# Performance work log

Hardware: AMD Instinct MI355X
Metric: run time of the kernel (lower is better)

Reference implementation:

```python
import jax, jax.numpy as jnp
import numpy as np

B, L, D_BERT, D_PROJ, N_SPANS, HIDDEN, EXTRA = 128, 512, 1024, 64, 3, 512, 17
BN_EPS = 1e-5


def setup_inputs() -> dict:
    key = jax.random.key(0)
    ks = jax.random.split(key, 20)
    inp = {
        "bert_outputs": jax.random.normal(ks[0], (B, L, D_BERT), jnp.float32),
        "offsets": jnp.sort(jax.random.randint(ks[1], (B, N_SPANS, 2), 0, L), axis=-1),
        "in_urls": jax.random.uniform(ks[2], (B, 3), jnp.float32),
        "other_feats": jax.random.normal(ks[3], (B, 14), jnp.float32),
        # context conv (Conv1d: out=64, in=1024, k=3)
        "conv_w": jax.random.normal(ks[4], (D_PROJ, D_BERT, 3), jnp.float32) * 0.02,
        "conv_b": jnp.zeros((D_PROJ,), jnp.float32),
        # span extractor global attention Linear(64 -> 1)
        "att_w": jax.random.normal(ks[5], (D_PROJ,), jnp.float32) * 0.1,
        "att_b": jnp.zeros((), jnp.float32),
        # BatchNorm1d(192) in eval mode (running stats)
        "bn1_g": jnp.ones((D_PROJ * 3,), jnp.float32),
        "bn1_b": jnp.zeros((D_PROJ * 3,), jnp.float32),
        "bn1_m": jax.random.normal(ks[6], (D_PROJ * 3,), jnp.float32) * 0.1,
        "bn1_v": jax.random.uniform(ks[7], (D_PROJ * 3,), jnp.float32, 0.5, 1.5),
        # Linear(192 -> 512), kaiming
        "fc_w": jax.random.normal(ks[8], (HIDDEN, D_PROJ * 3), jnp.float32) * np.sqrt(2.0 / (D_PROJ * 3)),
        "fc_b": jnp.zeros((HIDDEN,), jnp.float32),
        # BatchNorm1d(512)
        "bn2_g": jnp.ones((HIDDEN,), jnp.float32),
        "bn2_b": jnp.zeros((HIDDEN,), jnp.float32),
        "bn2_m": jax.random.normal(ks[9], (HIDDEN,), jnp.float32) * 0.1,
        "bn2_v": jax.random.uniform(ks[10], (HIDDEN,), jnp.float32, 0.5, 1.5),
        # new_last_layer Linear(512+17 -> 3)
        "last_w": jax.random.normal(ks[11], (3, HIDDEN + EXTRA), jnp.float32) * 0.05,
        "last_b": jnp.zeros((3,), jnp.float32),
    }
    return inp


def _bn_eval(x, g, b, m, v):
    return (x - m) * jax.lax.rsqrt(v + BN_EPS) * g + b


def reference(bert_outputs, offsets, in_urls, other_feats, conv_w, conv_b,
              att_w, att_b, bn1_g, bn1_b, bn1_m, bn1_v, fc_w, fc_b,
              bn2_g, bn2_b, bn2_m, bn2_v, last_w, last_b):
    # Conv1d over sequence: [B,L,Dbert] -> [B,L,64], padding preserves length
    x = jnp.transpose(bert_outputs, (0, 2, 1))                      # [B, C_in, L]
    conv = jax.lax.conv_general_dilated(
        x, conv_w, window_strides=(1,), padding=[(1, 1)],
        dimension_numbers=("NCH", "OIH", "NCH"))
    conv = jnp.transpose(conv + conv_b[None, :, None], (0, 2, 1))   # [B, L, 64]

    # SelfAttentiveSpanExtractor: per-token logits, masked softmax within span, weighted sum
    logits = jnp.einsum("bld,d->bl", conv, att_w) + att_b           # [B, L]
    pos = jnp.arange(L)
    starts = offsets[..., 0][..., None]                             # [B, S, 1]
    ends = offsets[..., 1][..., None]
    span_mask = (pos[None, None, :] >= starts) & (pos[None, None, :] <= ends)  # [B,S,L]
    masked_logits = jnp.where(span_mask, logits[:, None, :], -1e9)
    attn = jax.nn.softmax(masked_logits, axis=-1)                   # [B, S, L]
    span_emb = jnp.einsum("bsl,bld->bsd", attn, conv)               # [B, S, 64]
    extracted = span_emb.reshape(span_emb.shape[0], -1)             # [B, 192]

    # fc: BN -> Linear -> ReLU -> BN -> Dropout(eval=identity)
    h = _bn_eval(extracted, bn1_g, bn1_b, bn1_m, bn1_v)
    h = jax.nn.relu(h @ fc_w.T + fc_b)
    h = _bn_eval(h, bn2_g, bn2_b, bn2_m, bn2_v)

    cat = jnp.concatenate([h, in_urls, other_feats], axis=1)        # [B, 529]
    return cat @ last_w.T + last_b                                  # [B, 3]
```

## Files before the change

### kernel.cpp

```cpp
#include <hip/hip_runtime.h>


typedef _Float16 f16x8 __attribute__((ext_vector_type(8)));
typedef _Float16 f16x4 __attribute__((ext_vector_type(4)));
typedef float    f32x16 __attribute__((ext_vector_type(16)));

#define B_      128
#define L_      512
#define DBERT   1024
#define DPROJ   64
#define NSPANS  3
#define HIDDEN  512
#define KSTEPS  32
#define BM      32
#define AROWS   34
#define ASTR    1032

__global__ __launch_bounds__(256)
void pack_w_kernel(const float* __restrict__ Wc, _Float16* __restrict__ Bp) {
    int idx = blockIdx.x * 256 + threadIdx.x;
    if (idx >= 384 * 64) return;
    int lane = idx & 63;
    int f    = idx >> 6;
    int ch   = f & 1;
    int ks   = (f >> 1) & 1;
    int t    = (f >> 2) % 3;
    int kb   = (f >> 2) / 3;
    int o     = ch * 32 + (lane & 31);
    int kbase = kb * 32 + ks * 16 + ((lane >> 5) << 3);
    f16x8 v;
    #pragma unroll
    for (int j = 0; j < 8; ++j)
        v[j] = (_Float16)Wc[(size_t)o * (DBERT * 3) + (size_t)(kbase + j) * 3 + t];
    *(f16x8*)(Bp + (size_t)idx * 8) = v;
}

__global__ __launch_bounds__(256, 2)
void conv_gemm_kernel(const float* __restrict__ X, const _Float16* __restrict__ Bp,
                      const float* __restrict__ cb, const float* __restrict__ aw,
                      const float* __restrict__ ab_p,
                      float* __restrict__ Y, float* __restrict__ Lg) {
    __shared__ __align__(16) char shraw[AROWS * ASTR * 2];
    __shared__ float loglds[2][BM];

    _Float16* As = (_Float16*)shraw;

    const int tid  = threadIdx.x;
    const int wv   = tid >> 6;
    const int lane = tid & 63;
    const int ch   = wv & 1;
    const int ks   = wv >> 1;
    const int m0   = blockIdx.x * BM;
    const int l0   = m0 & (L_ - 1);
    const int g0   = m0 - l0;

    f16x8 bcur[3], bnxt[3];
    #pragma unroll
    for (int t = 0; t < 3; ++t)
        bcur[t] = *(const f16x8*)(Bp + ((size_t)((t * 2 + ks) * 2 + ch) * 64 + lane) * 8);

    #pragma unroll
    for (int base = 0; base < 34; base += 8) {
        const int n = (base + 8 <= 34) ? 8 : (34 - base);
        float4 v[8];
        #pragma unroll
        for (int i = 0; i < 8; ++i) {
            if (i < n) {
                int l = l0 - 1 + base + i;
                v[i] = make_float4(0.f, 0.f, 0.f, 0.f);
                if (l >= 0 && l < L_)
                    v[i] = *(const float4*)(X + (size_t)(g0 + l) * DBERT + tid * 4);
            }
        }
        #pragma unroll
        for (int i = 0; i < 8; ++i) {
            if (i < n) {
                f16x4 h = {(_Float16)v[i].x, (_Float16)v[i].y,
                           (_Float16)v[i].z, (_Float16)v[i].w};
                *(f16x4*)(&As[(base + i) * ASTR + tid * 4]) = h;
            }
        }
    }
    __syncthreads();

    f32x16 acc = {};
    #pragma unroll 2
    for (int kb = 0; kb < KSTEPS; ++kb) {
        if (kb + 1 < KSTEPS) {
            #pragma unroll
            for (int t = 0; t < 3; ++t)
                bnxt[t] = *(const f16x8*)(
                    Bp + ((size_t)((((kb + 1) * 3 + t) * 2 + ks) * 2 + ch) * 64 + lane) * 8);
        }
        f16x8 afr[3];
        const int kboff = kb * 32 + ks * 16 + ((lane >> 5) << 3);
        #pragma unroll
        for (int t = 0; t < 3; ++t)
            afr[t] = *(const f16x8*)(&As[((lane & 31) + t) * ASTR + kboff]);
        #pragma unroll
        for (int t = 0; t < 3; ++t)
            acc = __builtin_amdgcn_mfma_f32_32x32x16_f16(afr[t], bcur[t], acc, 0, 0, 0);
        #pragma unroll
        for (int t = 0; t < 3; ++t) bcur[t] = bnxt[t];
    }

    __syncthreads();
    float* red = (float*)shraw;
    if (ks == 1) {
        #pragma unroll
        for (int i = 0; i < 16; ++i) red[(ch * 64 + lane) * 16 + i] = acc[i];
    }
    __syncthreads();
    if (ks == 0) {
        const int col = ch * 32 + (lane & 31);
        const float cbv = cb[col];
        const float awv = aw[col];
        const int rbase = (lane >> 5) << 2;
        #pragma unroll
        for (int i = 0; i < 16; ++i) {
            float c = acc[i] + red[(ch * 64 + lane) * 16 + i] + cbv;
            int row = (i & 3) + 8 * (i >> 2) + rbase;
            Y[(size_t)(m0 + row) * DPROJ + col] = c;
            float p = c * awv;
            p += __shfl_xor(p, 1);  p += __shfl_xor(p, 2);
            p += __shfl_xor(p, 4);  p += __shfl_xor(p, 8);
            p += __shfl_xor(p, 16);
            if ((lane & 31) == 0) loglds[ch][row] = p;
        }
    }
    __syncthreads();
    if (tid < BM)
        Lg[m0 + tid] = loglds[0][tid] + loglds[1][tid] + ab_p[0];
}

__global__ __launch_bounds__(256)
void span_emb_kernel(const float* __restrict__ conv, const float* __restrict__ Lg,
                     const int* __restrict__ offs, float* __restrict__ emb) {
    __shared__ float logits[L_];
    __shared__ float red[8];
    __shared__ float part[256];

    const int bs   = blockIdx.x;
    const int b    = bs / NSPANS;
    const int sp   = bs - b * NSPANS;
    const int tid  = threadIdx.x;
    const int lane = tid & 63;
    const int wv   = tid >> 6;

    if (tid < 128)
        *(float4*)(&logits[tid * 4]) = *(const float4*)(Lg + (size_t)b * L_ + tid * 4);
    __syncthreads();

    const int st = offs[b * (NSPANS * 2) + sp * 2 + 0];
    const int en = offs[b * (NSPANS * 2) + sp * 2 + 1];

    float mx = -1e30f;
    for (int l = st + tid; l <= en; l += 256) mx = fmaxf(mx, logits[l]);
    #pragma unroll
    for (int off = 32; off >= 1; off >>= 1) mx = fmaxf(mx, __shfl_xor(mx, off));
    if (lane == 0) red[wv] = mx;
    __syncthreads();
    mx = fmaxf(fmaxf(red[0], red[1]), fmaxf(red[2], red[3]));
    __syncthreads();

    float sm = 0.f;
    for (int l = st + tid; l <= en; l += 256) sm += __expf(logits[l] - mx);
    #pragma unroll
    for (int off = 32; off >= 1; off >>= 1) sm += __shfl_xor(sm, off);
    if (lane == 0) red[wv] = sm;
    __syncthreads();
    const float denom = red[0] + red[1] + red[2] + red[3];

    float a = 0.f;
    for (int l = st + wv; l <= en; l += 4)
        a += __expf(logits[l] - mx) * conv[((size_t)b * L_ + l) * DPROJ + lane];
    part[tid] = a;
    __syncthreads();
    if (tid < DPROJ)
        emb[(size_t)bs * DPROJ + tid] =
            (part[tid] + part[64 + tid] + part[128 + tid] + part[192 + tid]) / denom;
}

__global__ __launch_bounds__(256)
void span_fc_kernel(const float* __restrict__ emb_in,
                    const float* __restrict__ in_urls, const float* __restrict__ other,
                    const float* __restrict__ bn1_g, const float* __restrict__ bn1_b,
                    const float* __restrict__ bn1_m, const float* __restrict__ bn1_v,
                    const float* __restrict__ fc_w, const float* __restrict__ fc_b,
                    const float* __restrict__ bn2_g, const float* __restrict__ bn2_b,
                    const float* __restrict__ bn2_m, const float* __restrict__ bn2_v,
                    const float* __restrict__ last_w, const float* __restrict__ last_b,
                    float* __restrict__ out) {
    __shared__ float emb[NSPANS * DPROJ];
    __shared__ float hbuf[HIDDEN];

    const int b    = blockIdx.x;
    const int tid  = threadIdx.x;
    const int lane = tid & 63;
    const int wv   = tid >> 6;

    if (tid < NSPANS * DPROJ) {
        float e = emb_in[(size_t)b * (NSPANS * DPROJ) + tid];
        emb[tid] = (e - bn1_m[tid]) * rsqrtf(bn1_v[tid] + 1e-5f) * bn1_g[tid] + bn1_b[tid];
    }
    __syncthreads();

    #pragma unroll
    for (int q = 0; q < 2; ++q) {
        const int j = tid + q * 256;
        const float* wrow = fc_w + (size_t)j * (NSPANS * DPROJ);
        float s = fc_b[j];
        #pragma unroll 8
        for (int i = 0; i < NSPANS * DPROJ; ++i) s += wrow[i] * emb[i];
        s = fmaxf(s, 0.f);
        hbuf[j] = (s - bn2_m[j]) * rsqrtf(bn2_v[j] + 1e-5f) * bn2_g[j] + bn2_b[j];
    }
    __syncthreads();

    if (wv < 3) {
        const float* lw = last_w + wv * (HIDDEN + 17);
        float s = 0.f;
        for (int i = lane; i < HIDDEN + 17; i += 64) {
            float f;
            if (i < HIDDEN)          f = hbuf[i];
            else if (i < HIDDEN + 3) f = in_urls[b * 3 + (i - HIDDEN)];
            else                     f = other[b * 14 + (i - HIDDEN - 3)];
            s += lw[i] * f;
        }
        #pragma unroll
        for (int off = 32; off >= 1; off >>= 1) s += __shfl_xor(s, off);
        if (lane == 0) out[b * 3 + wv] = s + last_b[wv];
    }
}

extern "C" void kernel_launch(void* const* d_in, const int* in_sizes, int n_in,
                              void* d_out, int out_size, void* d_ws, size_t ws_size,
                              hipStream_t stream) {
    const float* bert    = (const float*)d_in[0];
    const int*   offs    = (const int*)d_in[1];
    const float* in_urls = (const float*)d_in[2];
    const float* other   = (const float*)d_in[3];
    const float* conv_w  = (const float*)d_in[4];
    const float* conv_b  = (const float*)d_in[5];
    const float* att_w   = (const float*)d_in[6];
    const float* att_b   = (const float*)d_in[7];
    const float* bn1_g   = (const float*)d_in[8];
    const float* bn1_b   = (const float*)d_in[9];
    const float* bn1_m   = (const float*)d_in[10];
    const float* bn1_v   = (const float*)d_in[11];
    const float* fc_w    = (const float*)d_in[12];
    const float* fc_b    = (const float*)d_in[13];
    const float* bn2_g   = (const float*)d_in[14];
    const float* bn2_b   = (const float*)d_in[15];
    const float* bn2_m   = (const float*)d_in[16];
    const float* bn2_v   = (const float*)d_in[17];
    const float* last_w  = (const float*)d_in[18];
    const float* last_b  = (const float*)d_in[19];

    _Float16* Bp      = (_Float16*)d_ws;
    float*    convout = (float*)((char*)d_ws + 393216);
    float*    logits  = (float*)((char*)d_ws + 393216 + (size_t)B_ * L_ * DPROJ * 4);
    float*    emb     = (float*)((char*)d_ws + 393216 + (size_t)B_ * L_ * DPROJ * 4 + 262144);

    hipLaunchKernelGGL(pack_w_kernel, dim3(96), dim3(256), 0, stream, conv_w, Bp);
    hipLaunchKernelGGL(conv_gemm_kernel, dim3((B_ * L_) / BM), dim3(256), 0, stream,
                       bert, Bp, conv_b, att_w, att_b, convout, logits);
    hipLaunchKernelGGL(span_emb_kernel, dim3(B_ * NSPANS), dim3(256), 0, stream,
                       convout, logits, offs, emb);
    hipLaunchKernelGGL(span_fc_kernel, dim3(B_), dim3(256), 0, stream,
                       emb, in_urls, other,
                       bn1_g, bn1_b, bn1_m, bn1_v, fc_w, fc_b,
                       bn2_g, bn2_b, bn2_m, bn2_v, last_w, last_b,
                       (float*)d_out);
}
```

Measured before the change: 152.1 us.

## Load conv GEMM A operands straight from global memory, dropping LDS staging

```diff
diff --git a/kernel.cpp b/kernel.cpp
--- a/kernel.cpp
+++ b/kernel.cpp
@@ -2,7 +2,6 @@
 
 
 typedef _Float16 f16x8 __attribute__((ext_vector_type(8)));
-typedef _Float16 f16x4 __attribute__((ext_vector_type(4)));
 typedef float    f32x16 __attribute__((ext_vector_type(16)));
 
 #define B_      128
@@ -11,10 +10,7 @@
 #define DPROJ   64
 #define NSPANS  3
 #define HIDDEN  512
-#define KSTEPS  32
-#define BM      32
-#define AROWS   34
-#define ASTR    1032
+#define KK      64
 
 __global__ __launch_bounds__(256)
 void pack_w_kernel(const float* __restrict__ Wc, _Float16* __restrict__ Bp) {
@@ -23,11 +19,10 @@
     int lane = idx & 63;
     int f    = idx >> 6;
     int ch   = f & 1;
-    int ks   = (f >> 1) & 1;
-    int t    = (f >> 2) % 3;
-    int kb   = (f >> 2) / 3;
+    int t    = (f >> 1) % 3;
+    int kk   = (f >> 1) / 3;
     int o     = ch * 32 + (lane & 31);
-    int kbase = kb * 32 + ks * 16 + ((lane >> 5) << 3);
+    int kbase = kk * 16 + ((lane >> 5) << 3);
     f16x8 v;
     #pragma unroll
     for (int j = 0; j < 8; ++j)
@@ -35,101 +30,86 @@
     *(f16x8*)(Bp + (size_t)idx * 8) = v;
 }
 
-__global__ __launch_bounds__(256, 2)
+__global__ __launch_bounds__(256, 4)
 void conv_gemm_kernel(const float* __restrict__ X, const _Float16* __restrict__ Bp,
                       const float* __restrict__ cb, const float* __restrict__ aw,
-                      const float* __restrict__ ab_p,
+                      const float* __restrict__ ab_p, const float* __restrict__ zp,
                       float* __restrict__ Y, float* __restrict__ Lg) {
-    __shared__ __align__(16) char shraw[AROWS * ASTR * 2];
-    __shared__ float loglds[2][BM];
-
-    _Float16* As = (_Float16*)shraw;
+    __shared__ float loglds[2][64];
 
     const int tid  = threadIdx.x;
     const int wv   = tid >> 6;
     const int lane = tid & 63;
+    const int rg   = wv >> 1;
     const int ch   = wv & 1;
-    const int ks   = wv >> 1;
-    const int m0   = blockIdx.x * BM;
+    const int m0   = blockIdx.x * 64;
     const int l0   = m0 & (L_ - 1);
     const int g0   = m0 - l0;
-
-    f16x8 bcur[3], bnxt[3];
-    #pragma unroll
-    for (int t = 0; t < 3; ++t)
-        bcur[t] = *(const f16x8*)(Bp + ((size_t)((t * 2 + ks) * 2 + ch) * 64 + lane) * 8);
-
-    #pragma unroll
-    for (int base = 0; base < 34; base += 8) {
-        const int n = (base + 8 <= 34) ? 8 : (34 - base);
-        float4 v[8];
-        #pragma unroll
-        for (int i = 0; i < 8; ++i) {
-            if (i < n) {
-                int l = l0 - 1 + base + i;
-                v[i] = make_float4(0.f, 0.f, 0.f, 0.f);
-                if (l >= 0 && l < L_)
-                    v[i] = *(const float4*)(X + (size_t)(g0 + l) * DBERT + tid * 4);
-            }
-        }
-        #pragma unroll
-        for (int i = 0; i < 8; ++i) {
-            if (i < n) {
-                f16x4 h = {(_Float16)v[i].x, (_Float16)v[i].y,
-                           (_Float16)v[i].z, (_Float16)v[i].w};
-                *(f16x4*)(&As[(base + i) * ASTR + tid * 4]) = h;
-            }
-        }
-    }
-    __syncthreads();
+    const int r    = rg * 32 + (lane & 31);
+    const int koct = (lane >> 5) << 3;
+
+    const float* ap[3];
+    #pragma unroll
+    for (int t = 0; t < 3; ++t) {
+        int l = l0 + r + t - 1;
+        ap[t] = (l >= 0 && l < L_) ? (X + (size_t)(g0 + l) * DBERT + koct)
+                                   : (zp + koct);
+    }
+    const _Float16* bp = Bp + (size_t)ch * 512 + (size_t)lane * 8;
+
+    float4 a0[3][2], a1[3][2];
+    f16x8  b0[3], b1[3];
+    #pragma unroll
+    for (int t = 0; t < 3; ++t) {
+        a0[t][0] = *(const float4*)(ap[t]);
+        a0[t][1] = *(const float4*)(ap[t] + 4);
+        b0[t]    = *(const f16x8*)(bp + t * 1024);
+    }
 
     f32x16 acc = {};
     #pragma unroll 2
-    for (int kb = 0; kb < KSTEPS; ++kb) {
-        if (kb + 1 < KSTEPS) {
+    for (int kk = 0; kk < KK; ++kk) {
+        if (kk + 1 < KK) {
             #pragma unroll
-            for (int t = 0; t < 3; ++t)
-                bnxt[t] = *(const f16x8*)(
-                    Bp + ((size_t)((((kb + 1) * 3 + t) * 2 + ks) * 2 + ch) * 64 + lane) * 8);
-        }
-        f16x8 afr[3];
-        const int kboff = kb * 32 + ks * 16 + ((lane >> 5) << 3);
+            for (int t = 0; t < 3; ++t) {
+                const float* p = ap[t] + (kk + 1) * 16;
+                a1[t][0] = *(const float4*)(p);
+                a1[t][1] = *(const float4*)(p + 4);
+                b1[t]    = *(const f16x8*)(bp + (size_t)(kk + 1) * 3072 + t * 1024);
+            }
+        }
         #pragma unroll
-        for (int t = 0; t < 3; ++t)
-            afr[t] = *(const f16x8*)(&As[((lane & 31) + t) * ASTR + kboff]);
+        for (int t = 0; t < 3; ++t) {
+            f16x8 h;
+            h[0] = (_Float16)a0[t][0].x; h[1] = (_Float16)a0[t][0].y;
+            h[2] = (_Float16)a0[t][0].z; h[3] = (_Float16)a0[t][0].w;
+            h[4] = (_Float16)a0[t][1].x; h[5] = (_Float16)a0[t][1].y;
+            h[6] = (_Float16)a0[t][1].z; h[7] = (_Float16)a0[t][1].w;
+            acc = __builtin_amdgcn_mfma_f32_32x32x16_f16(h, b0[t], acc, 0, 0, 0);
+        }
         #pragma unroll
-        for (int t = 0; t < 3; ++t)
-            acc = __builtin_amdgcn_mfma_f32_32x32x16_f16(afr[t], bcur[t], acc, 0, 0, 0);
-        #pragma unroll
-        for (int t = 0; t < 3; ++t) bcur[t] = bnxt[t];
-    }
-
-    __syncthreads();
-    float* red = (float*)shraw;
-    if (ks == 1) {
-        #pragma unroll
-        for (int i = 0; i < 16; ++i) red[(ch * 64 + lane) * 16 + i] = acc[i];
-    }
-    __syncthreads();
-    if (ks == 0) {
-        const int col = ch * 32 + (lane & 31);
-        const float cbv = cb[col];
-        const float awv = aw[col];
-        const int rbase = (lane >> 5) << 2;
-        #pragma unroll
-        for (int i = 0; i < 16; ++i) {
-            float c = acc[i] + red[(ch * 64 + lane) * 16 + i] + cbv;
-            int row = (i & 3) + 8 * (i >> 2) + rbase;
-            Y[(size_t)(m0 + row) * DPROJ + col] = c;
-            float p = c * awv;
-            p += __shfl_xor(p, 1);  p += __shfl_xor(p, 2);
-            p += __shfl_xor(p, 4);  p += __shfl_xor(p, 8);
-            p += __shfl_xor(p, 16);
-            if ((lane & 31) == 0) loglds[ch][row] = p;
-        }
-    }
-    __syncthreads();
-    if (tid < BM)
+        for (int t = 0; t < 3; ++t) {
+            a0[t][0] = a1[t][0]; a0[t][1] = a1[t][1]; b0[t] = b1[t];
+        }
+    }
+
+    const int   col = ch * 32 + (lane & 31);
+    const float cbv = cb[col];
+    const float awv = aw[col];
+    const int rbase = (lane >> 5) << 2;
+    #pragma unroll
+    for (int i = 0; i < 16; ++i) {
+        float c = acc[i] + cbv;
+        int row = (i & 3) + 8 * (i >> 2) + rbase;
+        Y[(size_t)(m0 + rg * 32 + row) * DPROJ + col] = c;
+        float p = c * awv;
+        p += __shfl_xor(p, 1);  p += __shfl_xor(p, 2);
+        p += __shfl_xor(p, 4);  p += __shfl_xor(p, 8);
+        p += __shfl_xor(p, 16);
+        if ((lane & 31) == 0) loglds[ch][rg * 32 + row] = p;
+    }
+    __syncthreads();
+    if (tid < 64)
         Lg[m0 + tid] = loglds[0][tid] + loglds[1][tid] + ab_p[0];
 }
 
@@ -259,12 +239,14 @@
 
     _Float16* Bp      = (_Float16*)d_ws;
     float*    convout = (float*)((char*)d_ws + 393216);
-    float*    logits  = (float*)((char*)d_ws + 393216 + (size_t)B_ * L_ * DPROJ * 4);
-    float*    emb     = (float*)((char*)d_ws + 393216 + (size_t)B_ * L_ * DPROJ * 4 + 262144);
-
+    float*    logits  = (float*)((char*)d_ws + 17170432);
+    float*    emb     = (float*)((char*)d_ws + 17432576);
+    float*    zeros   = (float*)((char*)d_ws + 17530880);
+
+    hipMemsetAsync(zeros, 0, 4096, stream);
     hipLaunchKernelGGL(pack_w_kernel, dim3(96), dim3(256), 0, stream, conv_w, Bp);
-    hipLaunchKernelGGL(conv_gemm_kernel, dim3((B_ * L_) / BM), dim3(256), 0, stream,
-                       bert, Bp, conv_b, att_w, att_b, convout, logits);
+    hipLaunchKernelGGL(conv_gemm_kernel, dim3((B_ * L_) / 64), dim3(256), 0, stream,
+                       bert, Bp, conv_b, att_w, att_b, zeros, convout, logits);
     hipLaunchKernelGGL(span_emb_kernel, dim3(B_ * NSPANS), dim3(256), 0, stream,
                        convout, logits, offs, emb);
     hipLaunchKernelGGL(span_fc_kernel, dim3(B_), dim3(256), 0, stream,
```

New measurement: 262.2 us. +72.4%, slower.
